# Kernel tuning notes

Measured on AMD Instinct MI355X. Metric: run time of the kernel, lower is better.

The kernel has to match this reference:

```python
import jax, jax.numpy as jnp
import numpy as np

EPS = 1e-6
K_HOPS = 2  # SGConv K


def setup_inputs() -> dict:
    key = jax.random.key(0)
    k1, k2, k3, k4 = jax.random.split(key, 4)
    B, Kk, C, T = 32, 8, 64, 250
    E, H = 4096, 128
    x = jax.random.normal(k1, (B, Kk, C, T), dtype=jnp.float32)
    edge_index = jax.random.randint(k2, (2, E), 0, C, dtype=jnp.int64)
    edge_weights = jax.random.uniform(k3, (E,), dtype=jnp.float32)
    W = jax.random.normal(k4, (H, Kk * T), dtype=jnp.float32) * 0.02
    b = jnp.zeros((H,), dtype=jnp.float32)
    return {"x": x, "edge_index": edge_index, "edge_weights": edge_weights, "W": W, "b": b}


def reference(x, edge_index, edge_weights, W, b):
    B, Kk, C, T = x.shape
    N = C  # nodes
    x = x.reshape(B, N, Kk * T)  # (B, N, F)

    # clamp non-positive edge weights to epsilon (mirrors in-place .data clamp)
    w = jnp.where(edge_weights <= 0, EPS, edge_weights)

    # gcn_norm with self loops (fill value 1.0)
    src, dst = edge_index[0], edge_index[1]
    loop = jnp.arange(N, dtype=edge_index.dtype)
    src = jnp.concatenate([src, loop])
    dst = jnp.concatenate([dst, loop])
    w = jnp.concatenate([w, jnp.ones((N,), w.dtype)])
    deg = jnp.zeros((N,), w.dtype).at[dst].add(w)
    dinv = jnp.where(deg > 0, deg ** -0.5, jnp.zeros_like(deg))
    norm = dinv[src] * w * dinv[dst]  # (E+N,)

    # K hops of gather -> weight -> scatter-add aggregation
    for _ in range(K_HOPS):
        msg = x[:, src, :] * norm[None, :, None]        # (B, E+N, F)
        x = jnp.zeros_like(x).at[:, dst, :].add(msg)    # (B, N, F)

    # final linear: y = x @ W^T + b
    return jnp.einsum('bnf,hf->bnh', x, W) + b
```

## Files before the change

kernel.cpp:

```cpp
#include <hip/hip_runtime.h>
#include <hip/hip_bf16.h>

#define EPSW 1e-6f

typedef __attribute__((ext_vector_type(4))) float floatx4;
typedef __attribute__((ext_vector_type(2))) unsigned int uintx2;
typedef __attribute__((ext_vector_type(4))) unsigned int uintx4;
typedef __attribute__((ext_vector_type(8))) short shortx8;

__device__ __forceinline__ unsigned short f2bf(float f) {
    unsigned int u = __float_as_uint(f);
    u = (u + 0x7fffu + ((u >> 16) & 1u)) >> 16;
    return (unsigned short)u;
}

__device__ __forceinline__ float bf2f(unsigned short b) {
    return __uint_as_float((unsigned int)b << 16);
}

__device__ __forceinline__ unsigned int pk2(float lo, float hi) {
    return (unsigned int)f2bf(lo) | ((unsigned int)f2bf(hi) << 16);
}

__device__ __forceinline__ void gl_lds16(const void* g, void* l) {
    __builtin_amdgcn_global_load_lds(
        (const __attribute__((address_space(1))) unsigned int*)g,
        (__attribute__((address_space(3))) unsigned int*)l, 16, 0, 0);
}

__global__ __launch_bounds__(512) void prep(const float* __restrict__ W,
                                            const int* __restrict__ ei,
                                            const float* __restrict__ ew,
                                            const float* __restrict__ bias,
                                            unsigned short* __restrict__ wt,
                                            float* __restrict__ Mt,
                                            float* __restrict__ y) {
    __shared__ float sA[4096 + 128];
    const int bid = blockIdx.x;
    const int t   = threadIdx.x;

    if (bid < 16) {
#pragma unroll
        for (int i = 0; i < 4; ++i) {
            const int G  = bid * 2048 + i * 512 + t;
            const int kg = G >> 7;
            const int h  = G & 127;
            const int k  = kg * 8;
            floatx4 v0 = (floatx4){0.f, 0.f, 0.f, 0.f};
            floatx4 v1 = (floatx4){0.f, 0.f, 0.f, 0.f};
            if (k < 2000) {
                v0 = *(const floatx4*)(W + (size_t)h * 2000 + k);
                v1 = *(const floatx4*)(W + (size_t)h * 2000 + k + 4);
            }
            unsigned short* p = wt + ((size_t)kg * 128 + h) * 8;
            p[0] = f2bf(v0.x); p[1] = f2bf(v0.y); p[2] = f2bf(v0.z); p[3] = f2bf(v0.w);
            p[4] = f2bf(v1.x); p[5] = f2bf(v1.y); p[6] = f2bf(v1.z); p[7] = f2bf(v1.w);
        }
    } else if (bid < 20) {
        const int bb = bid - 16;
        float* A    = sA;
        float* deg  = sA + 4096;
        float* dinv = deg + 64;
        if (t < 64) deg[t] = 1.0f;
        for (int i = t; i < 4096; i += 512) A[i] = 0.0f;
        __syncthreads();
        const int* srcp = ei;
        const int* dstp = ei + 4096;
#pragma unroll
        for (int i = 0; i < 8; ++i) {
            const int e = i * 512 + t;
            float w = ew[e];
            w = (w <= 0.0f) ? EPSW : w;
            atomicAdd(&deg[dstp[e]], w);
        }
        __syncthreads();
        if (t < 64) dinv[t] = 1.0f / sqrtf(deg[t]);
        __syncthreads();
#pragma unroll
        for (int i = 0; i < 8; ++i) {
            const int e = i * 512 + t;
            float w = ew[e];
            w = (w <= 0.0f) ? EPSW : w;
            const int s = srcp[e], d = dstp[e];
            atomicAdd(&A[d * 64 + s], dinv[s] * w * dinv[d]);
        }
        if (t < 64) atomicAdd(&A[t * 64 + t], dinv[t] * dinv[t]);
        __syncthreads();
        const int c  = t & 63;
        const int n0 = bb * 16 + (t >> 6);
        const int n1 = n0 + 8;
        float s0 = 0.0f, s1 = 0.0f;
#pragma unroll 8
        for (int k = 0; k < 64; ++k) {
            const float akc = A[k * 64 + c];
            s0 += A[n0 * 64 + k] * akc;
            s1 += A[n1 * 64 + k] * akc;
        }
        Mt[c * 64 + n0] = s0;
        Mt[c * 64 + n1] = s1;
    } else {
        const floatx4 bv = *(const floatx4*)(bias + (t & 31) * 4);
#pragma unroll
        for (int i = 0; i < 16; ++i) {
            const int idx4 = (bid - 20) * 8192 + i * 512 + t;
            *(floatx4*)(y + (size_t)idx4 * 4) = bv;
        }
    }
}

__global__ __launch_bounds__(256) void gemm_fused(
        const float* __restrict__ x,
        const unsigned short* __restrict__ wt,
        const float* __restrict__ Mtg,
        float* __restrict__ y) {
    __shared__ __align__(16) unsigned char smem[2][24576];
    __shared__ __align__(16) unsigned char mg[16384];
    const int t    = threadIdx.x;
    const int wave = t >> 6, lane = t & 63;
    const int m = lane & 15, q = lane >> 4;
    const int bid   = blockIdx.x;
    const int ks    = bid >> 5;
    const int bb    = bid & 31;
    const int rbase = bb * 64;
    const int kg0   = ks * 32;

    const int kgl = lane >> 3;
    const int rr0 = wave * 8 + (lane & 7);

    floatx4 acc[4][2];
#pragma unroll
    for (int rt = 0; rt < 4; ++rt)
#pragma unroll
        for (int hh = 0; hh < 2; ++hh)
            acc[rt][hh] = (floatx4){0.f, 0.f, 0.f, 0.f};

    floatx4 va0, va1, vb0, vb1;

#define LOAD_A(c)                                                             \
    {                                                                         \
        const int k_ = ks * 256 + (c) * 64 + kgl * 8;                         \
        const float* px_ = x + (size_t)(rbase + rr0) * 2000 + k_;             \
        if (k_ < 2000) {                                                      \
            va0 = *(const floatx4*)px_;                                       \
            va1 = *(const floatx4*)(px_ + 4);                                 \
            vb0 = *(const floatx4*)(px_ + 64000);                             \
            vb1 = *(const floatx4*)(px_ + 64004);                             \
        } else {                                                              \
            va0 = va1 = vb0 = vb1 = (floatx4){0.f, 0.f, 0.f, 0.f};            \
        }                                                                     \
    }

#define WRITE_A(c)                                                            \
    {                                                                         \
        unsigned char* sb_ = smem[(c) & 1];                                   \
        uintx4 g0_, g1_;                                                      \
        g0_.x = pk2(va0.x, va0.y); g0_.y = pk2(va0.z, va0.w);                 \
        g0_.z = pk2(va1.x, va1.y); g0_.w = pk2(va1.z, va1.w);                 \
        g1_.x = pk2(vb0.x, vb0.y); g1_.y = pk2(vb0.z, vb0.w);                 \
        g1_.z = pk2(vb1.x, vb1.y); g1_.w = pk2(vb1.z, vb1.w);                 \
        *(uintx4*)(sb_ + kgl * 1024 + rr0 * 16) = g0_;                        \
        *(uintx4*)(sb_ + kgl * 1024 + (rr0 + 32) * 16) = g1_;                 \
    }

#define ISSUE_B(c)                                                            \
    {                                                                         \
        unsigned char* sb_ = smem[(c) & 1];                                   \
        const int ckg_ = kg0 + (c) * 8;                                       \
        for (int j = wave; j < 16; j += 4) {                                  \
            const int kb_ = j >> 1, hf_ = j & 1;                              \
            gl_lds16(wt + ((size_t)(ckg_ + kb_) * 128 + hf_ * 64 + lane) * 8, \
                     sb_ + 8192 + kb_ * 2048 + hf_ * 1024);                   \
        }                                                                     \
    }

    LOAD_A(0);
    ISSUE_B(0);

#pragma unroll
    for (int s = 0; s < 2; ++s) {
        const int g  = t * 2 + s;
        const int kg = g >> 6, n = g & 63;
        float v[8];
#pragma unroll
        for (int j = 0; j < 8; ++j) v[j] = Mtg[(kg * 8 + j) * 64 + n];
        unsigned short hb[8];
#pragma unroll
        for (int j = 0; j < 8; ++j) hb[j] = f2bf(v[j]);
        uintx4 wh, wl;
        wh.x = (unsigned)hb[0] | ((unsigned)hb[1] << 16);
        wh.y = (unsigned)hb[2] | ((unsigned)hb[3] << 16);
        wh.z = (unsigned)hb[4] | ((unsigned)hb[5] << 16);
        wh.w = (unsigned)hb[6] | ((unsigned)hb[7] << 16);
        wl.x = pk2(v[0] - bf2f(hb[0]), v[1] - bf2f(hb[1]));
        wl.y = pk2(v[2] - bf2f(hb[2]), v[3] - bf2f(hb[3]));
        wl.z = pk2(v[4] - bf2f(hb[4]), v[5] - bf2f(hb[5]));
        wl.w = pk2(v[6] - bf2f(hb[6]), v[7] - bf2f(hb[7]));
        *(uintx4*)(mg + g * 16)        = wh;
        *(uintx4*)(mg + 8192 + g * 16) = wl;
    }

    for (int c = 0; c < 4; ++c) {
        __builtin_amdgcn_s_waitcnt(0);
        WRITE_A(c);
        if (c < 3) {
            LOAD_A(c + 1);
            ISSUE_B(c + 1);
        }
        __syncthreads();
        const unsigned char* sb = smem[c & 1];
#pragma unroll
        for (int p = 0; p < 2; ++p) {
            shortx8 a[4];
#pragma unroll
            for (int rt = 0; rt < 4; ++rt)
                a[rt] = *(const shortx8*)(sb + (p * 4 + q) * 1024 + (rt * 16 + m) * 16);
            shortx8 bbf[2];
#pragma unroll
            for (int hh = 0; hh < 2; ++hh)
                bbf[hh] = *(const shortx8*)(sb + 8192 + (p * 4 + q) * 2048 +
                                            ((wave + hh * 4) * 16 + m) * 16);
#pragma unroll
            for (int rt = 0; rt < 4; ++rt)
#pragma unroll
                for (int hh = 0; hh < 2; ++hh)
                    acc[rt][hh] = __builtin_amdgcn_mfma_f32_16x16x32_bf16(
                        a[rt], bbf[hh], acc[rt][hh], 0, 0, 0);
        }
        __syncthreads();
    }
#undef LOAD_A
#undef WRITE_A
#undef ISSUE_B

    unsigned char* zhi = smem[0];
    unsigned char* zlo = smem[1];
#pragma unroll
    for (int rt = 0; rt < 4; ++rt) {
        const int kg  = rt * 2 + (q >> 1);
        const int off = (q & 1) * 8;
#pragma unroll
        for (int hh = 0; hh < 2; ++hh) {
            const int h = (wave + hh * 4) * 16 + m;
            const floatx4 a = acc[rt][hh];
            const unsigned short h0 = f2bf(a.x), h1 = f2bf(a.y),
                                 h2 = f2bf(a.z), h3 = f2bf(a.w);
            uintx2 wh, wl;
            wh.x = (unsigned)h0 | ((unsigned)h1 << 16);
            wh.y = (unsigned)h2 | ((unsigned)h3 << 16);
            wl.x = pk2(a.x - bf2f(h0), a.y - bf2f(h1));
            wl.y = pk2(a.z - bf2f(h2), a.w - bf2f(h3));
            const int base = (kg * 129 + h) * 16 + off;
            *(uintx2*)(zhi + base) = wh;
            *(uintx2*)(zlo + base) = wl;
        }
    }
    __syncthreads();

    floatx4 acc2[4][2];
#pragma unroll
    for (int nt = 0; nt < 4; ++nt)
#pragma unroll
        for (int hh = 0; hh < 2; ++hh)
            acc2[nt][hh] = (floatx4){0.f, 0.f, 0.f, 0.f};

#pragma unroll
    for (int kst = 0; kst < 2; ++kst) {
        shortx8 ah[4], al[4];
#pragma unroll
        for (int nt = 0; nt < 4; ++nt) {
            const int ga = ((kst * 4 + q) * 64 + nt * 16 + m) * 16;
            ah[nt] = *(const shortx8*)(mg + ga);
            al[nt] = *(const shortx8*)(mg + 8192 + ga);
        }
        shortx8 bh[2], bl[2];
#pragma unroll
        for (int hh = 0; hh < 2; ++hh) {
            const int gb = ((kst * 4 + q) * 129 + (wave + hh * 4) * 16 + m) * 16;
            bh[hh] = *(const shortx8*)(zhi + gb);
            bl[hh] = *(const shortx8*)(zlo + gb);
        }
#pragma unroll
        for (int nt = 0; nt < 4; ++nt)
#pragma unroll
            for (int hh = 0; hh < 2; ++hh) {
                acc2[nt][hh] = __builtin_amdgcn_mfma_f32_16x16x32_bf16(
                    ah[nt], bh[hh], acc2[nt][hh], 0, 0, 0);
                acc2[nt][hh] = __builtin_amdgcn_mfma_f32_16x16x32_bf16(
                    ah[nt], bl[hh], acc2[nt][hh], 0, 0, 0);
                acc2[nt][hh] = __builtin_amdgcn_mfma_f32_16x16x32_bf16(
                    al[nt], bh[hh], acc2[nt][hh], 0, 0, 0);
            }
    }

    float* yb = y + (size_t)bb * 8192;
#pragma unroll
    for (int nt = 0; nt < 4; ++nt)
#pragma unroll
        for (int hh = 0; hh < 2; ++hh) {
            const int h = (wave + hh * 4) * 16 + m;
#pragma unroll
            for (int v = 0; v < 4; ++v) {
                const int n = nt * 16 + q * 4 + v;
                atomicAdd(yb + n * 128 + h, acc2[nt][hh][v]);
            }
        }
}

extern "C" void kernel_launch(void* const* d_in, const int* in_sizes, int n_in,
                              void* d_out, int out_size, void* d_ws, size_t ws_size,
                              hipStream_t stream) {
    const float* x    = (const float*)d_in[0];
    const int*   ei   = (const int*)d_in[1];
    const float* ew   = (const float*)d_in[2];
    const float* W    = (const float*)d_in[3];
    const float* bias = (const float*)d_in[4];
    float* y = (float*)d_out;

    float* Mt = (float*)d_ws;
    unsigned short* wt = (unsigned short*)(Mt + 4096);

    prep<<<28, 512, 0, stream>>>(W, ei, ew, bias, wt, Mt, y);
    gemm_fused<<<256, 256, 0, stream>>>(x, wt, Mt, y);
}
```

Baseline: 95.05 us.

## Reduce K-split partials via last-block workspace reduction instead of atomics

The before code applied the 64x64 graph operator to each K-split partial of x·W^T and atomically added the results into a bias-initialised output. Now each block writes its fp32 partial to a workspace, and the last of the eight K-split blocks for a batch (found with a counter) sums the partials. That block then applies the graph operator once with split-bf16 MFMA and stores the output plus bias directly. This drops the bias-fill blocks in prep, the output atomics and the per-split graph GEMM, and the block-to-tile mapping is remapped. The cost is extra global traffic for the partials, a serial tail in the last block, and reliance on threadfence plus counter ordering.

```diff
diff --git a/kernel.cpp b/kernel.cpp
--- a/kernel.cpp
+++ b/kernel.cpp
@@ -4,7 +4,6 @@
 #define EPSW 1e-6f
 
 typedef __attribute__((ext_vector_type(4))) float floatx4;
-typedef __attribute__((ext_vector_type(2))) unsigned int uintx2;
 typedef __attribute__((ext_vector_type(4))) unsigned int uintx4;
 typedef __attribute__((ext_vector_type(8))) short shortx8;
 
@@ -31,15 +30,15 @@
 __global__ __launch_bounds__(512) void prep(const float* __restrict__ W,
                                             const int* __restrict__ ei,
                                             const float* __restrict__ ew,
-                                            const float* __restrict__ bias,
                                             unsigned short* __restrict__ wt,
                                             float* __restrict__ Mt,
-                                            float* __restrict__ y) {
+                                            int* __restrict__ cnt) {
     __shared__ float sA[4096 + 128];
     const int bid = blockIdx.x;
     const int t   = threadIdx.x;
 
     if (bid < 16) {
+        if (bid == 0 && t < 32) cnt[t] = 0;
 #pragma unroll
         for (int i = 0; i < 4; ++i) {
             const int G  = bid * 2048 + i * 512 + t;
@@ -56,7 +55,7 @@
             p[0] = f2bf(v0.x); p[1] = f2bf(v0.y); p[2] = f2bf(v0.z); p[3] = f2bf(v0.w);
             p[4] = f2bf(v1.x); p[5] = f2bf(v1.y); p[6] = f2bf(v1.z); p[7] = f2bf(v1.w);
         }
-    } else if (bid < 20) {
+    } else {
         const int bb = bid - 16;
         float* A    = sA;
         float* deg  = sA + 4096;
@@ -98,13 +97,6 @@
         }
         Mt[c * 64 + n0] = s0;
         Mt[c * 64 + n1] = s1;
-    } else {
-        const floatx4 bv = *(const floatx4*)(bias + (t & 31) * 4);
-#pragma unroll
-        for (int i = 0; i < 16; ++i) {
-            const int idx4 = (bid - 20) * 8192 + i * 512 + t;
-            *(floatx4*)(y + (size_t)idx4 * 4) = bv;
-        }
     }
 }
 
@@ -112,15 +104,19 @@
         const float* __restrict__ x,
         const unsigned short* __restrict__ wt,
         const float* __restrict__ Mtg,
+        const float* __restrict__ bias,
+        float* __restrict__ zp,
+        int* __restrict__ cnt,
         float* __restrict__ y) {
     __shared__ __align__(16) unsigned char smem[2][24576];
     __shared__ __align__(16) unsigned char mg[16384];
+    __shared__ int lastS;
     const int t    = threadIdx.x;
     const int wave = t >> 6, lane = t & 63;
     const int m = lane & 15, q = lane >> 4;
     const int bid   = blockIdx.x;
-    const int ks    = bid >> 5;
-    const int bb    = bid & 31;
+    const int bb    = (bid & 7) | ((bid >> 6) << 3);
+    const int ks    = (bid >> 3) & 7;
     const int rbase = bb * 64;
     const int kg0   = ks * 32;
 
@@ -175,10 +171,93 @@
 
     LOAD_A(0);
     ISSUE_B(0);
-
-#pragma unroll
-    for (int s = 0; s < 2; ++s) {
-        const int g  = t * 2 + s;
+    for (int c = 0; c < 4; ++c) {
+        __builtin_amdgcn_s_waitcnt(0);
+        WRITE_A(c);
+        if (c < 3) {
+            LOAD_A(c + 1);
+            ISSUE_B(c + 1);
+        }
+        __syncthreads();
+        const unsigned char* sb = smem[c & 1];
+#pragma unroll
+        for (int p = 0; p < 2; ++p) {
+            shortx8 a[4];
+#pragma unroll
+            for (int rt = 0; rt < 4; ++rt)
+                a[rt] = *(const shortx8*)(sb + (p * 4 + q) * 1024 + (rt * 16 + m) * 16);
+            shortx8 bbf[2];
+#pragma unroll
+            for (int hh = 0; hh < 2; ++hh)
+                bbf[hh] = *(const shortx8*)(sb + 8192 + (p * 4 + q) * 2048 +
+                                            ((wave + hh * 4) * 16 + m) * 16);
+#pragma unroll
+            for (int rt = 0; rt < 4; ++rt)
+#pragma unroll
+                for (int hh = 0; hh < 2; ++hh)
+                    acc[rt][hh] = __builtin_amdgcn_mfma_f32_16x16x32_bf16(
+                        a[rt], bbf[hh], acc[rt][hh], 0, 0, 0);
+        }
+        __syncthreads();
+    }
+#undef LOAD_A
+#undef WRITE_A
+#undef ISSUE_B
+
+    float* zslice = zp + ((size_t)bb * 8 + ks) * 8192;
+#pragma unroll
+    for (int rt = 0; rt < 4; ++rt)
+#pragma unroll
+        for (int hh = 0; hh < 2; ++hh) {
+            const int h = (wave + hh * 4) * 16 + m;
+#pragma unroll
+            for (int v = 0; v < 4; ++v) {
+                const int n = rt * 16 + q * 4 + v;
+                zslice[n * 128 + h] = acc[rt][hh][v];
+            }
+        }
+
+    __threadfence();
+    __syncthreads();
+    if (t == 0) lastS = (atomicAdd(&cnt[bb], 1) == 7);
+    __syncthreads();
+    if (!lastS) return;
+    __threadfence();
+
+    unsigned char* zhi = smem[0];
+    unsigned char* zlo = smem[1];
+    const float* zb = zp + (size_t)bb * 65536;
+#pragma unroll
+    for (int i = 0; i < 4; ++i) {
+        const int kg = i * 2 + (t >> 7);
+        const int h  = t & 127;
+        float s[8];
+#pragma unroll
+        for (int j = 0; j < 8; ++j) s[j] = 0.0f;
+        for (int ksx = 0; ksx < 8; ++ksx) {
+            const float* p = zb + ksx * 8192 + kg * 1024 + h;
+#pragma unroll
+            for (int j = 0; j < 8; ++j) s[j] += p[j * 128];
+        }
+        unsigned short hb[8];
+#pragma unroll
+        for (int j = 0; j < 8; ++j) hb[j] = f2bf(s[j]);
+        uintx4 wh, wl;
+        wh.x = (unsigned)hb[0] | ((unsigned)hb[1] << 16);
+        wh.y = (unsigned)hb[2] | ((unsigned)hb[3] << 16);
+        wh.z = (unsigned)hb[4] | ((unsigned)hb[5] << 16);
+        wh.w = (unsigned)hb[6] | ((unsigned)hb[7] << 16);
+        wl.x = pk2(s[0] - bf2f(hb[0]), s[1] - bf2f(hb[1]));
+        wl.y = pk2(s[2] - bf2f(hb[2]), s[3] - bf2f(hb[3]));
+        wl.z = pk2(s[4] - bf2f(hb[4]), s[5] - bf2f(hb[5]));
+        wl.w = pk2(s[6] - bf2f(hb[6]), s[7] - bf2f(hb[7]));
+        *(uintx4*)(zhi + (kg * 129 + h) * 16) = wh;
+        *(uintx4*)(zlo + (kg * 129 + h) * 16) = wl;
+    }
+
+#pragma unroll
+    for (int sg = 0; sg < 2; ++sg) {
+        const int g  = t * 2 + sg;
         const int kg = g >> 6, n = g & 63;
         float v[8];
 #pragma unroll
@@ -198,62 +277,6 @@
         *(uintx4*)(mg + g * 16)        = wh;
         *(uintx4*)(mg + 8192 + g * 16) = wl;
     }
-
-    for (int c = 0; c < 4; ++c) {
-        __builtin_amdgcn_s_waitcnt(0);
-        WRITE_A(c);
-        if (c < 3) {
-            LOAD_A(c + 1);
-            ISSUE_B(c + 1);
-        }
-        __syncthreads();
-        const unsigned char* sb = smem[c & 1];
-#pragma unroll
-        for (int p = 0; p < 2; ++p) {
-            shortx8 a[4];
-#pragma unroll
-            for (int rt = 0; rt < 4; ++rt)
-                a[rt] = *(const shortx8*)(sb + (p * 4 + q) * 1024 + (rt * 16 + m) * 16);
-            shortx8 bbf[2];
-#pragma unroll
-            for (int hh = 0; hh < 2; ++hh)
-                bbf[hh] = *(const shortx8*)(sb + 8192 + (p * 4 + q) * 2048 +
-                                            ((wave + hh * 4) * 16 + m) * 16);
-#pragma unroll
-            for (int rt = 0; rt < 4; ++rt)
-#pragma unroll
-                for (int hh = 0; hh < 2; ++hh)
-                    acc[rt][hh] = __builtin_amdgcn_mfma_f32_16x16x32_bf16(
-                        a[rt], bbf[hh], acc[rt][hh], 0, 0, 0);
-        }
-        __syncthreads();
-    }
-#undef LOAD_A
-#undef WRITE_A
-#undef ISSUE_B
-
-    unsigned char* zhi = smem[0];
-    unsigned char* zlo = smem[1];
-#pragma unroll
-    for (int rt = 0; rt < 4; ++rt) {
-        const int kg  = rt * 2 + (q >> 1);
-        const int off = (q & 1) * 8;
-#pragma unroll
-        for (int hh = 0; hh < 2; ++hh) {
-            const int h = (wave + hh * 4) * 16 + m;
-            const floatx4 a = acc[rt][hh];
-            const unsigned short h0 = f2bf(a.x), h1 = f2bf(a.y),
-                                 h2 = f2bf(a.z), h3 = f2bf(a.w);
-            uintx2 wh, wl;
-            wh.x = (unsigned)h0 | ((unsigned)h1 << 16);
-            wh.y = (unsigned)h2 | ((unsigned)h3 << 16);
-            wl.x = pk2(a.x - bf2f(h0), a.y - bf2f(h1));
-            wl.y = pk2(a.z - bf2f(h2), a.w - bf2f(h3));
-            const int base = (kg * 129 + h) * 16 + off;
-            *(uintx2*)(zhi + base) = wh;
-            *(uintx2*)(zlo + base) = wl;
-        }
-    }
     __syncthreads();
 
     floatx4 acc2[4][2];
@@ -297,11 +320,12 @@
     for (int nt = 0; nt < 4; ++nt)
 #pragma unroll
         for (int hh = 0; hh < 2; ++hh) {
-            const int h = (wave + hh * 4) * 16 + m;
+            const int h  = (wave + hh * 4) * 16 + m;
+            const float bv = bias[h];
 #pragma unroll
             for (int v = 0; v < 4; ++v) {
                 const int n = nt * 16 + q * 4 + v;
-                atomicAdd(yb + n * 128 + h, acc2[nt][hh][v]);
+                yb[n * 128 + h] = bv + acc2[nt][hh][v];
             }
         }
 }
@@ -316,9 +340,11 @@
     const float* bias = (const float*)d_in[4];
     float* y = (float*)d_out;
 
-    float* Mt = (float*)d_ws;
+    float* zp = (float*)d_ws;
+    float* Mt = zp + 2097152;
     unsigned short* wt = (unsigned short*)(Mt + 4096);
-
-    prep<<<28, 512, 0, stream>>>(W, ei, ew, bias, wt, Mt, y);
-    gemm_fused<<<256, 256, 0, stream>>>(x, wt, Mt, y);
-}
+    int* cnt = (int*)(wt + 262144);
+
+    prep<<<20, 512, 0, stream>>>(W, ei, ew, wt, Mt, cnt);
+    gemm_fused<<<256, 256, 0, stream>>>(x, wt, Mt, bias, zp, cnt, y);
+}
```

New measurement: 121.5 us. 1.28x slower.
